# Kernel tuning notes

Hardware: AMD Instinct MI355X
Metric: run time of the kernel (lower is better)

The kernel has to match this reference:

```python
import jax, jax.numpy as jnp
import numpy as np

B, HN, N1, DIM = 4096, 16, 192, 256
EPS = 1e-5


def _xavier(key, fan_out, fan_in):
    limit = np.sqrt(6.0 / (fan_in + fan_out)).astype(np.float32)
    return jax.random.uniform(key, (fan_out, fan_in), jnp.float32, -limit, limit)


def setup_inputs() -> dict:
    key = jax.random.key(0)
    k_rgb, k_tir, k_idx, k_w1, k_w2 = jax.random.split(key, 5)
    attn_rgb_weight = jax.random.uniform(k_rgb, (B, HN, N1), jnp.float32)
    attn_tir_weight = jax.random.uniform(k_tir, (B, HN, N1), jnp.float32)
    # unique, sorted indices per batch into [0, DIM) (scatter with duplicate
    # indices is nondeterministic in torch, so we keep them unique)
    idx = jax.vmap(lambda k: jax.random.permutation(k, DIM)[:N1])(
        jax.random.split(k_idx, B))
    global_index_s = jnp.sort(idx, axis=-1).astype(jnp.int32)
    return {
        "attn_rgb_weight": attn_rgb_weight,
        "attn_tir_weight": attn_tir_weight,
        "global_index_s": global_index_s,
        "ln_g": jnp.ones((2 * DIM,), jnp.float32),
        "ln_b": jnp.zeros((2 * DIM,), jnp.float32),
        "W1": _xavier(k_w1, DIM, 2 * DIM),   # Linear(512 -> 256), torch (out,in)
        "b1": jnp.zeros((DIM,), jnp.float32),
        "W2": _xavier(k_w2, 2 * DIM, DIM),   # Linear(256 -> 512)
        "b2": jnp.zeros((2 * DIM,), jnp.float32),
    }


def reference(attn_rgb_weight, attn_tir_weight, global_index_s,
              ln_g, ln_b, W1, b1, W2, b2):
    b, hn, n1 = attn_rgb_weight.shape
    idx = global_index_s[:, None, :]                     # [B, 1, N1]
    bi = jnp.arange(b)[:, None, None]                    # [B, 1, 1]
    hi = jnp.arange(hn)[None, :, None]                   # [1, hn, 1]
    # scatter sparse attention weights into dense [B, hn, DIM] buffers
    vex_rgb = jnp.zeros((b, hn, DIM), attn_rgb_weight.dtype)
    vex_rgb = vex_rgb.at[bi, hi, idx].set(attn_rgb_weight)
    vex_tir = jnp.zeros((b, hn, DIM), attn_tir_weight.dtype)
    vex_tir = vex_tir.at[bi, hi, idx].set(attn_tir_weight)
    vex = jnp.concatenate([vex_rgb, vex_tir], axis=-1)   # [B, hn, 2*DIM]
    # LayerNorm(2*DIM) -> Linear -> ReLU -> Linear -> Sigmoid
    mu = jnp.mean(vex, axis=-1, keepdims=True)
    var = jnp.mean(jnp.square(vex - mu), axis=-1, keepdims=True)
    x = (vex - mu) * jax.lax.rsqrt(var + EPS) * ln_g + ln_b
    h = jax.nn.relu(jnp.einsum('bhe,de->bhd', x, W1) + b1)
    o = jax.nn.sigmoid(jnp.einsum('bhd,ed->bhe', h, W2) + b2)  # [B, hn, 2*DIM]
    # gather back via index
    idx_full = jnp.broadcast_to(idx, (b, hn, n1))
    out_rgb = jnp.take_along_axis(o[:, :, :DIM], idx_full, axis=-1)
    out_tir = jnp.take_along_axis(o[:, :, DIM:], idx_full, axis=-1)
    return (out_rgb, out_tir)
```

## Files before the change

kernel.cpp:

```cpp
#include <hip/hip_runtime.h>
#include <stdint.h>

#define NJ 192
#define OUT_HALF 12582912

#define XS 520
#define HS 264
#define OS 516

#define W1_OFF 33280
#define H_OFF  49664
#define ARENA  66560

typedef __attribute__((ext_vector_type(4))) float    f32x4;
typedef __attribute__((ext_vector_type(4))) int      i32x4;
typedef __attribute__((ext_vector_type(4))) uint32_t u32x4;
typedef __attribute__((ext_vector_type(8))) short    bf16x8;

__device__ __forceinline__ float bf2f(short u) {
    union { float f; uint32_t i; } c;
    c.i = ((uint32_t)(uint16_t)u) << 16;
    return c.f;
}
__device__ __forceinline__ uint32_t cvt_pk_bf16(float lo, float hi) {
    uint32_t r;
    asm("v_cvt_pk_bf16_f32 %0, %1, %2" : "=v"(r) : "v"(lo), "v"(hi));
    return r;
}
__device__ __forceinline__ void gload16(const void* g, void* l) {
    __builtin_amdgcn_global_load_lds(
        (const __attribute__((address_space(1))) uint32_t*)g,
        (__attribute__((address_space(3))) uint32_t*)l, 16, 0, 0);
}

__global__ __launch_bounds__(256)
void pack_weights(const float* __restrict__ W1, const float* __restrict__ W2,
                  short* __restrict__ ws) {
    int id = blockIdx.x * 256 + threadIdx.x;
    const float* src;
    short* dst;
    if (id < 16384) {
        int c = id >> 10, u = id & 1023;
        int nt = u >> 6, lane = u & 63;
        src = W1 + (nt * 16 + (lane & 15)) * 512 + c * 32 + (lane >> 4) * 8;
        dst = ws + id * 8;
    } else {
        int id2 = id - 16384;
        int c = id2 >> 11, u = id2 & 2047;
        int nt = u >> 6, lane = u & 63;
        src = W2 + (nt * 16 + (lane & 15)) * 256 + c * 32 + (lane >> 4) * 8;
        dst = ws + 131072 + id2 * 8;
    }
    f32x4 a = *(const f32x4*)src;
    f32x4 b = *(const f32x4*)(src + 4);
    u32x4 o;
    o[0] = cvt_pk_bf16(a[0], a[1]);
    o[1] = cvt_pk_bf16(a[2], a[3]);
    o[2] = cvt_pk_bf16(b[0], b[1]);
    o[3] = cvt_pk_bf16(b[2], b[3]);
    *(u32x4*)dst = o;
}

__global__ __launch_bounds__(512, 4)
void fused_mlp(const float* __restrict__ rgb,
               const float* __restrict__ tir,
               const int*  __restrict__ gidx,
               const float* __restrict__ ln_g,
               const float* __restrict__ ln_b,
               const short* __restrict__ P1,
               const float* __restrict__ b1,
               const short* __restrict__ P2,
               const float* __restrict__ b2,
               float* __restrict__ out)
{
    __shared__ __attribute__((aligned(16))) char arena[ARENA];
    short* sX  = (short*)arena;
    short* sW1 = (short*)(arena + W1_OFF);
    short* sH  = (short*)(arena + H_OFF);
    short* sW2 = (short*)arena;
    float* sO  = (float*)arena;

    const int tid  = threadIdx.x;
    const int blk  = blockIdx.x;
    const int row0 = blk * 32;
    const int b0   = blk * 2;
    const int wave = tid >> 6;
    const int lane = tid & 63;
    const int lr   = lane & 15;
    const int quad = lane >> 4;
    const int mw   = wave & 1;
    const int nw   = wave >> 1;

    const char* P1b = (const char*)P1;
    const char* P2b = (const char*)P2;
    char* w1dst = arena + W1_OFF + wave * 1024;
    char* w2dst = arena + wave * 1024;

    #pragma unroll
    for (int k = 0; k < 2; ++k)
        gload16(P1b + (k * 512 + tid) * 16, w1dst + k * 8192);

    {
        u32x4* xz = (u32x4*)sX;
        for (int u = tid; u < 2080; u += 512) xz[u] = (u32x4){0u, 0u, 0u, 0u};
    }
    __syncthreads();

    i32x4 ivs[3];
    #pragma unroll
    for (int it = 0; it < 3; ++it) {
        int p = (it * 512 + tid) * 4;
        int r = p / NJ;
        int j = p - r * NJ;
        ivs[it] = *(const i32x4*)&gidx[(b0 + (r >> 4)) * NJ + j];
        f32x4 vr = *(const f32x4*)&rgb[(row0 + r) * NJ + j];
        f32x4 vt = *(const f32x4*)&tir[(row0 + r) * NJ + j];
        short* xr = sX + r * XS;
        #pragma unroll
        for (int e = 0; e < 4; ++e) {
            uint32_t pk = cvt_pk_bf16(vr[e], vt[e]);
            xr[ivs[it][e]]       = (short)pk;
            xr[256 + ivs[it][e]] = (short)(pk >> 16);
        }
    }
    __syncthreads();

    {
        int r = tid >> 4, sub = tid & 15;
        short* xr = sX + r * XS + sub * 32;
        float s = 0.f, ss = 0.f;
        #pragma unroll
        for (int t = 0; t < 4; ++t) {
            bf16x8 v8 = *(bf16x8*)(xr + t * 8);
            #pragma unroll
            for (int e = 0; e < 8; ++e) { float v = bf2f(v8[e]); s += v; ss += v * v; }
        }
        s += __shfl_xor(s, 1, 16);  ss += __shfl_xor(ss, 1, 16);
        s += __shfl_xor(s, 2, 16);  ss += __shfl_xor(ss, 2, 16);
        s += __shfl_xor(s, 4, 16);  ss += __shfl_xor(ss, 4, 16);
        s += __shfl_xor(s, 8, 16);  ss += __shfl_xor(ss, 8, 16);
        float mu  = s * (1.f / 512.f);
        float var = ss * (1.f / 512.f) - mu * mu;
        float rs  = rsqrtf(var + 1e-5f);
        const float* gp = ln_g + sub * 32;
        const float* bp = ln_b + sub * 32;
        #pragma unroll
        for (int t = 0; t < 4; ++t) {
            bf16x8 v8 = *(bf16x8*)(xr + t * 8);
            f32x4 g0 = *(const f32x4*)(gp + t * 8);
            f32x4 g1 = *(const f32x4*)(gp + t * 8 + 4);
            f32x4 c0 = *(const f32x4*)(bp + t * 8);
            f32x4 c1 = *(const f32x4*)(bp + t * 8 + 4);
            float y0 = (bf2f(v8[0]) - mu) * rs * g0[0] + c0[0];
            float y1 = (bf2f(v8[1]) - mu) * rs * g0[1] + c0[1];
            float y2 = (bf2f(v8[2]) - mu) * rs * g0[2] + c0[2];
            float y3 = (bf2f(v8[3]) - mu) * rs * g0[3] + c0[3];
            float y4 = (bf2f(v8[4]) - mu) * rs * g1[0] + c1[0];
            float y5 = (bf2f(v8[5]) - mu) * rs * g1[1] + c1[1];
            float y6 = (bf2f(v8[6]) - mu) * rs * g1[2] + c1[2];
            float y7 = (bf2f(v8[7]) - mu) * rs * g1[3] + c1[3];
            u32x4 w;
            w[0] = cvt_pk_bf16(y0, y1);
            w[1] = cvt_pk_bf16(y2, y3);
            w[2] = cvt_pk_bf16(y4, y5);
            w[3] = cvt_pk_bf16(y6, y7);
            *(u32x4*)(xr + t * 8) = w;
        }
    }

    f32x4 acc1[4];
    #pragma unroll
    for (int i = 0; i < 4; ++i) acc1[i] = (f32x4){0.f, 0.f, 0.f, 0.f};

    const short* xrow   = sX + (mw * 16 + lr) * XS + quad * 8;
    const short* wfrag1 = sW1 + (nw * 4 * 64 + lane) * 8;

    for (int c = 0; c < 16; ++c) {
        __syncthreads();
        bf16x8 a = *(const bf16x8*)(xrow + c * 32);
        #pragma unroll
        for (int i = 0; i < 4; ++i) {
            bf16x8 b = *(const bf16x8*)(wfrag1 + i * 512);
            acc1[i] = __builtin_amdgcn_mfma_f32_16x16x32_bf16(a, b, acc1[i], 0, 0, 0);
        }
        __syncthreads();
        if (c < 15) {
            #pragma unroll
            for (int k = 0; k < 2; ++k)
                gload16(P1b + (c + 1) * 16384 + (k * 512 + tid) * 16, w1dst + k * 8192);
        }
    }

    #pragma unroll
    for (int k = 0; k < 4; ++k)
        gload16(P2b + (k * 512 + tid) * 16, w2dst + k * 8192);

    #pragma unroll
    for (int i = 0; i < 4; ++i) {
        int col = (nw * 4 + i) * 16 + lr;
        float bias = b1[col];
        #pragma unroll
        for (int rr = 0; rr < 4; ++rr) {
            int row = mw * 16 + quad * 4 + rr;
            float h = fmaxf(acc1[i][rr] + bias, 0.f);
            sH[row * HS + col] = (short)cvt_pk_bf16(h, h);
        }
    }

    f32x4 acc2[8];
    #pragma unroll
    for (int i = 0; i < 8; ++i) acc2[i] = (f32x4){0.f, 0.f, 0.f, 0.f};

    const short* hrow   = sH + (mw * 16 + lr) * HS + quad * 8;
    const short* wfrag2 = sW2 + (nw * 8 * 64 + lane) * 8;

    for (int c = 0; c < 8; ++c) {
        __syncthreads();
        bf16x8 a = *(const bf16x8*)(hrow + c * 32);
        #pragma unroll
        for (int i = 0; i < 8; ++i) {
            bf16x8 b = *(const bf16x8*)(wfrag2 + i * 512);
            acc2[i] = __builtin_amdgcn_mfma_f32_16x16x32_bf16(a, b, acc2[i], 0, 0, 0);
        }
        __syncthreads();
        if (c < 7) {
            #pragma unroll
            for (int k = 0; k < 4; ++k)
                gload16(P2b + (c + 1) * 32768 + (k * 512 + tid) * 16, w2dst + k * 8192);
        }
    }

    #pragma unroll
    for (int i = 0; i < 8; ++i) {
        int col = (nw * 8 + i) * 16 + lr;
        float bias = b2[col];
        #pragma unroll
        for (int rr = 0; rr < 4; ++rr) {
            int row = mw * 16 + quad * 4 + rr;
            float x = acc2[i][rr] + bias;
            sO[row * OS + col] = 1.f / (1.f + __expf(-x));
        }
    }
    __syncthreads();

    #pragma unroll
    for (int it = 0; it < 3; ++it) {
        int p = (it * 512 + tid) * 4;
        int r = p / NJ;
        int j = p - r * NJ;
        const float* orow = sO + r * OS;
        f32x4 vr, vt;
        #pragma unroll
        for (int e = 0; e < 4; ++e) {
            vr[e] = orow[ivs[it][e]];
            vt[e] = orow[256 + ivs[it][e]];
        }
        *(f32x4*)&out[(row0 + r) * NJ + j]            = vr;
        *(f32x4*)&out[OUT_HALF + (row0 + r) * NJ + j] = vt;
    }
}

extern "C" void kernel_launch(void* const* d_in, const int* in_sizes, int n_in,
                              void* d_out, int out_size, void* d_ws, size_t ws_size,
                              hipStream_t stream) {
    const float* rgb  = (const float*)d_in[0];
    const float* tir  = (const float*)d_in[1];
    const int*   gidx = (const int*)d_in[2];
    const float* ln_g = (const float*)d_in[3];
    const float* ln_b = (const float*)d_in[4];
    const float* W1   = (const float*)d_in[5];
    const float* b1   = (const float*)d_in[6];
    const float* W2   = (const float*)d_in[7];
    const float* b2   = (const float*)d_in[8];
    float* out = (float*)d_out;
    short* wsp = (short*)d_ws;

    pack_weights<<<128, 256, 0, stream>>>(W1, W2, wsp);
    fused_mlp<<<2048, 512, 0, stream>>>(rgb, tir, gidx, ln_g, ln_b,
                                        wsp, b1, wsp + 131072, b2, out);
}
```

Measured before the change: 277.4 us.

## Fold LayerNorm into W1, double rows per block, register-cache X fragments

The LayerNorm affine (gamma, beta) and bias b1 are folded into the packed W1 and precomputed per-column vectors, so the kernel only computes per-row mean/rstd, applies them after the first GEMM, and skips the normalize-and-rewrite pass over X. Each block now handles 64 rows instead of 32, halving how often each block streams the weights, and holds the A fragments for GEMM1 in registers. Weight tiles are double-buffered in 8KB/16KB slots, and the W2 prefetch overlaps the tail of GEMM1. Output columns are interleaved rgb/tir so the gather reads float2 pairs. This raises register pressure (16 A fragments plus 16 accumulators) and computes the LN statistics from fp32 inputs before the bf16 rounding.

```diff
diff --git a/kernel.cpp b/kernel.cpp
--- a/kernel.cpp
+++ b/kernel.cpp
@@ -6,22 +6,22 @@
 
 #define XS 520
 #define HS 264
-#define OS 516
-
-#define W1_OFF 33280
-#define H_OFF  49664
-#define ARENA  66560
+#define OSD 516
+
+#define SLOTB  16384
+#define H_OFF  33280
+#define STAT_OFF 67072
+#define ARENA  67584
 
 typedef __attribute__((ext_vector_type(4))) float    f32x4;
+typedef __attribute__((ext_vector_type(2))) float    f32x2;
 typedef __attribute__((ext_vector_type(4))) int      i32x4;
 typedef __attribute__((ext_vector_type(4))) uint32_t u32x4;
 typedef __attribute__((ext_vector_type(8))) short    bf16x8;
 
-__device__ __forceinline__ float bf2f(short u) {
-    union { float f; uint32_t i; } c;
-    c.i = ((uint32_t)(uint16_t)u) << 16;
-    return c.f;
-}
+__device__ float g_u1[256];
+__device__ float g_v1[256];
+
 __device__ __forceinline__ uint32_t cvt_pk_bf16(float lo, float hi) {
     uint32_t r;
     asm("v_cvt_pk_bf16_f32 %0, %1, %2" : "=v"(r) : "v"(lo), "v"(hi));
@@ -35,228 +35,263 @@
 
 __global__ __launch_bounds__(256)
 void pack_weights(const float* __restrict__ W1, const float* __restrict__ W2,
-                  short* __restrict__ ws) {
+                  const float* __restrict__ ln_g, const float* __restrict__ ln_b,
+                  const float* __restrict__ b1, short* __restrict__ ws) {
+    if (blockIdx.x == 128) {
+        int d = threadIdx.x;
+        float u = b1[d], v = 0.f;
+        const float* wr = W1 + d * 512;
+        for (int e = 0; e < 512; e += 4) {
+            f32x4 w4 = *(const f32x4*)(wr + e);
+            f32x4 g4 = *(const f32x4*)(ln_g + e);
+            f32x4 l4 = *(const f32x4*)(ln_b + e);
+            #pragma unroll
+            for (int t = 0; t < 4; ++t) { v += w4[t] * g4[t]; u += w4[t] * l4[t]; }
+        }
+        g_u1[d] = u; g_v1[d] = v;
+        return;
+    }
     int id = blockIdx.x * 256 + threadIdx.x;
-    const float* src;
-    short* dst;
     if (id < 16384) {
-        int c = id >> 10, u = id & 1023;
-        int nt = u >> 6, lane = u & 63;
-        src = W1 + (nt * 16 + (lane & 15)) * 512 + c * 32 + (lane >> 4) * 8;
-        dst = ws + id * 8;
+        int u8 = id >> 9, w = id & 511;
+        int c = u8 >> 1, h = u8 & 1;
+        int t2 = w >> 6, lane = w & 63;
+        int nt = 2 * t2 + h;
+        int row = nt * 16 + (lane & 15);
+        int k0 = c * 16 + ((lane >> 4) << 2);
+        f32x4 a  = *(const f32x4*)(W1 + row * 512 + k0);
+        f32x4 b  = *(const f32x4*)(W1 + row * 512 + 256 + k0);
+        f32x4 ga = *(const f32x4*)(ln_g + k0);
+        f32x4 gb = *(const f32x4*)(ln_g + 256 + k0);
+        u32x4 o;
+        #pragma unroll
+        for (int t = 0; t < 4; ++t) o[t] = cvt_pk_bf16(a[t] * ga[t], b[t] * gb[t]);
+        *(u32x4*)(ws + id * 8) = o;
     } else {
         int id2 = id - 16384;
-        int c = id2 >> 11, u = id2 & 2047;
-        int nt = u >> 6, lane = u & 63;
-        src = W2 + (nt * 16 + (lane & 15)) * 256 + c * 32 + (lane >> 4) * 8;
-        dst = ws + 131072 + id2 * 8;
-    }
-    f32x4 a = *(const f32x4*)src;
-    f32x4 b = *(const f32x4*)(src + 4);
-    u32x4 o;
-    o[0] = cvt_pk_bf16(a[0], a[1]);
-    o[1] = cvt_pk_bf16(a[2], a[3]);
-    o[2] = cvt_pk_bf16(b[0], b[1]);
-    o[3] = cvt_pk_bf16(b[2], b[3]);
-    *(u32x4*)dst = o;
+        int u16 = id2 >> 10, w = id2 & 1023;
+        int c = u16 >> 1, h = u16 & 1;
+        int t2 = w >> 6, lane = w & 63;
+        int nt = 2 * t2 + h;
+        int rp = nt * 16 + (lane & 15);
+        int orow = (rp >> 1) + (rp & 1) * 256;
+        int k0 = c * 32 + ((lane >> 4) << 3);
+        f32x4 a = *(const f32x4*)(W2 + orow * 256 + k0);
+        f32x4 b = *(const f32x4*)(W2 + orow * 256 + k0 + 4);
+        u32x4 o;
+        o[0] = cvt_pk_bf16(a[0], a[1]);
+        o[1] = cvt_pk_bf16(a[2], a[3]);
+        o[2] = cvt_pk_bf16(b[0], b[1]);
+        o[3] = cvt_pk_bf16(b[2], b[3]);
+        *(u32x4*)(ws + 131072 + id2 * 8) = o;
+    }
 }
 
 __global__ __launch_bounds__(512, 4)
 void fused_mlp(const float* __restrict__ rgb,
                const float* __restrict__ tir,
                const int*  __restrict__ gidx,
-               const float* __restrict__ ln_g,
-               const float* __restrict__ ln_b,
                const short* __restrict__ P1,
-               const float* __restrict__ b1,
                const short* __restrict__ P2,
                const float* __restrict__ b2,
                float* __restrict__ out)
 {
     __shared__ __attribute__((aligned(16))) char arena[ARENA];
-    short* sX  = (short*)arena;
-    short* sW1 = (short*)(arena + W1_OFF);
-    short* sH  = (short*)(arena + H_OFF);
-    short* sW2 = (short*)arena;
-    float* sO  = (float*)arena;
+    short* sX    = (short*)arena;
+    short* sH    = (short*)(arena + H_OFF);
+    float* sStat = (float*)(arena + STAT_OFF);
+    float* sO    = (float*)arena;
 
     const int tid  = threadIdx.x;
     const int blk  = blockIdx.x;
-    const int row0 = blk * 32;
-    const int b0   = blk * 2;
+    const int row0 = blk * 64;
+    const int b0   = blk * 4;
     const int wave = tid >> 6;
     const int lane = tid & 63;
     const int lr   = lane & 15;
     const int quad = lane >> 4;
-    const int mw   = wave & 1;
-    const int nw   = wave >> 1;
+    const int mw   = wave & 3;
+    const int nw   = wave >> 2;
 
     const char* P1b = (const char*)P1;
     const char* P2b = (const char*)P2;
-    char* w1dst = arena + W1_OFF + wave * 1024;
-    char* w2dst = arena + wave * 1024;
-
-    #pragma unroll
-    for (int k = 0; k < 2; ++k)
-        gload16(P1b + (k * 512 + tid) * 16, w1dst + k * 8192);
 
     {
-        u32x4* xz = (u32x4*)sX;
-        for (int u = tid; u < 2080; u += 512) xz[u] = (u32x4){0u, 0u, 0u, 0u};
-    }
-    __syncthreads();
-
-    i32x4 ivs[3];
-    #pragma unroll
-    for (int it = 0; it < 3; ++it) {
-        int p = (it * 512 + tid) * 4;
-        int r = p / NJ;
-        int j = p - r * NJ;
-        ivs[it] = *(const i32x4*)&gidx[(b0 + (r >> 4)) * NJ + j];
-        f32x4 vr = *(const f32x4*)&rgb[(row0 + r) * NJ + j];
-        f32x4 vt = *(const f32x4*)&tir[(row0 + r) * NJ + j];
-        short* xr = sX + r * XS;
-        #pragma unroll
-        for (int e = 0; e < 4; ++e) {
-            uint32_t pk = cvt_pk_bf16(vr[e], vt[e]);
-            xr[ivs[it][e]]       = (short)pk;
-            xr[256 + ivs[it][e]] = (short)(pk >> 16);
+        uint32_t* xd = (uint32_t*)sX;
+        #pragma unroll
+        for (int i = 0; i < 8; ++i) {
+            int u = i * 512 + tid;
+            int r = u >> 6, g = u & 63;
+            *(u32x4*)(xd + r * 260 + g * 4) = (u32x4){0u, 0u, 0u, 0u};
         }
     }
     __syncthreads();
 
     {
-        int r = tid >> 4, sub = tid & 15;
-        short* xr = sX + r * XS + sub * 32;
+        int r = tid >> 3, sub = tid & 7;
+        int j0 = sub * 24;
+        uint32_t* xdw = (uint32_t*)(sX + r * XS);
+        const int*   gp = gidx + (b0 + (r >> 4)) * NJ + j0;
+        const float* rp = rgb + (row0 + r) * NJ + j0;
+        const float* tp = tir + (row0 + r) * NJ + j0;
         float s = 0.f, ss = 0.f;
         #pragma unroll
-        for (int t = 0; t < 4; ++t) {
-            bf16x8 v8 = *(bf16x8*)(xr + t * 8);
-            #pragma unroll
-            for (int e = 0; e < 8; ++e) { float v = bf2f(v8[e]); s += v; ss += v * v; }
-        }
-        s += __shfl_xor(s, 1, 16);  ss += __shfl_xor(ss, 1, 16);
-        s += __shfl_xor(s, 2, 16);  ss += __shfl_xor(ss, 2, 16);
-        s += __shfl_xor(s, 4, 16);  ss += __shfl_xor(ss, 4, 16);
-        s += __shfl_xor(s, 8, 16);  ss += __shfl_xor(ss, 8, 16);
+        for (int q = 0; q < 6; ++q) {
+            i32x4 iv = *(const i32x4*)(gp + q * 4);
+            f32x4 vr = *(const f32x4*)(rp + q * 4);
+            f32x4 vt = *(const f32x4*)(tp + q * 4);
+            #pragma unroll
+            for (int e = 0; e < 4; ++e) {
+                s  += vr[e] + vt[e];
+                ss += vr[e] * vr[e] + vt[e] * vt[e];
+                xdw[iv[e]] = cvt_pk_bf16(vr[e], vt[e]);
+            }
+        }
+        s  += __shfl_xor(s, 1, 8);  ss += __shfl_xor(ss, 1, 8);
+        s  += __shfl_xor(s, 2, 8);  ss += __shfl_xor(ss, 2, 8);
+        s  += __shfl_xor(s, 4, 8);  ss += __shfl_xor(ss, 4, 8);
         float mu  = s * (1.f / 512.f);
         float var = ss * (1.f / 512.f) - mu * mu;
         float rs  = rsqrtf(var + 1e-5f);
-        const float* gp = ln_g + sub * 32;
-        const float* bp = ln_b + sub * 32;
-        #pragma unroll
-        for (int t = 0; t < 4; ++t) {
-            bf16x8 v8 = *(bf16x8*)(xr + t * 8);
-            f32x4 g0 = *(const f32x4*)(gp + t * 8);
-            f32x4 g1 = *(const f32x4*)(gp + t * 8 + 4);
-            f32x4 c0 = *(const f32x4*)(bp + t * 8);
-            f32x4 c1 = *(const f32x4*)(bp + t * 8 + 4);
-            float y0 = (bf2f(v8[0]) - mu) * rs * g0[0] + c0[0];
-            float y1 = (bf2f(v8[1]) - mu) * rs * g0[1] + c0[1];
-            float y2 = (bf2f(v8[2]) - mu) * rs * g0[2] + c0[2];
-            float y3 = (bf2f(v8[3]) - mu) * rs * g0[3] + c0[3];
-            float y4 = (bf2f(v8[4]) - mu) * rs * g1[0] + c1[0];
-            float y5 = (bf2f(v8[5]) - mu) * rs * g1[1] + c1[1];
-            float y6 = (bf2f(v8[6]) - mu) * rs * g1[2] + c1[2];
-            float y7 = (bf2f(v8[7]) - mu) * rs * g1[3] + c1[3];
-            u32x4 w;
-            w[0] = cvt_pk_bf16(y0, y1);
-            w[1] = cvt_pk_bf16(y2, y3);
-            w[2] = cvt_pk_bf16(y4, y5);
-            w[3] = cvt_pk_bf16(y6, y7);
-            *(u32x4*)(xr + t * 8) = w;
-        }
-    }
-
-    f32x4 acc1[4];
-    #pragma unroll
-    for (int i = 0; i < 4; ++i) acc1[i] = (f32x4){0.f, 0.f, 0.f, 0.f};
-
-    const short* xrow   = sX + (mw * 16 + lr) * XS + quad * 8;
-    const short* wfrag1 = sW1 + (nw * 4 * 64 + lane) * 8;
-
-    for (int c = 0; c < 16; ++c) {
+        if (sub == 0) { sStat[2 * r] = rs; sStat[2 * r + 1] = mu * rs; }
+    }
+    __syncthreads();
+
+    bf16x8 a1[16];
+    {
+        const short* xr = sX + (mw * 16 + lr) * XS + quad * 8;
+        #pragma unroll
+        for (int c = 0; c < 16; ++c) a1[c] = *(const bf16x8*)(xr + c * 32);
+    }
+    __syncthreads();
+
+    gload16(P1b + 0 * 8192 + tid * 16, arena + 0       + wave * 1024);
+    gload16(P1b + 1 * 8192 + tid * 16, arena + SLOTB   + wave * 1024);
+    __syncthreads();
+
+    f32x4 acc1[8];
+    #pragma unroll
+    for (int i = 0; i < 8; ++i) acc1[i] = (f32x4){0.f, 0.f, 0.f, 0.f};
+
+    const short* wb = (const short*)arena + lane * 8;
+
+    #pragma unroll
+    for (int j = 0; j < 32; ++j) {
+        const int c = j >> 1, h = j & 1;
+        bf16x8 w0 = *(const bf16x8*)(wb + (j & 1) * 8192 + (nw * 4 + 0) * 512);
+        bf16x8 w1 = *(const bf16x8*)(wb + (j & 1) * 8192 + (nw * 4 + 1) * 512);
+        bf16x8 w2 = *(const bf16x8*)(wb + (j & 1) * 8192 + (nw * 4 + 2) * 512);
+        bf16x8 w3 = *(const bf16x8*)(wb + (j & 1) * 8192 + (nw * 4 + 3) * 512);
         __syncthreads();
-        bf16x8 a = *(const bf16x8*)(xrow + c * 32);
-        #pragma unroll
-        for (int i = 0; i < 4; ++i) {
-            bf16x8 b = *(const bf16x8*)(wfrag1 + i * 512);
-            acc1[i] = __builtin_amdgcn_mfma_f32_16x16x32_bf16(a, b, acc1[i], 0, 0, 0);
-        }
+        if (j <= 29) {
+            gload16(P1b + (j + 2) * 8192 + tid * 16,
+                    arena + (j & 1) * SLOTB + wave * 1024);
+        } else {
+            const int u = j - 30;
+            gload16(P2b + u * 16384 + tid * 16,
+                    arena + u * SLOTB + wave * 1024);
+            gload16(P2b + u * 16384 + 8192 + tid * 16,
+                    arena + u * SLOTB + 8192 + wave * 1024);
+        }
+        acc1[0 + h] = __builtin_amdgcn_mfma_f32_16x16x32_bf16(a1[c], w0, acc1[0 + h], 0, 0, 0);
+        acc1[2 + h] = __builtin_amdgcn_mfma_f32_16x16x32_bf16(a1[c], w1, acc1[2 + h], 0, 0, 0);
+        acc1[4 + h] = __builtin_amdgcn_mfma_f32_16x16x32_bf16(a1[c], w2, acc1[4 + h], 0, 0, 0);
+        acc1[6 + h] = __builtin_amdgcn_mfma_f32_16x16x32_bf16(a1[c], w3, acc1[6 + h], 0, 0, 0);
+    }
+
+    {
+        const int baserow = mw * 16 + quad * 4;
+        float rsv[4], mrs[4];
+        #pragma unroll
+        for (int rr = 0; rr < 4; ++rr) {
+            rsv[rr] = sStat[2 * (baserow + rr)];
+            mrs[rr] = sStat[2 * (baserow + rr) + 1];
+        }
+        #pragma unroll
+        for (int i = 0; i < 8; ++i) {
+            int col = (nw * 8 + i) * 16 + lr;
+            float u1c = g_u1[col], v1c = g_v1[col];
+            #pragma unroll
+            for (int rr = 0; rr < 4; ++rr) {
+                float hh = rsv[rr] * acc1[i][rr] + (u1c - mrs[rr] * v1c);
+                hh = fmaxf(hh, 0.f);
+                sH[(baserow + rr) * HS + col] = (short)cvt_pk_bf16(hh, hh);
+            }
+        }
+    }
+    __syncthreads();
+
+    f32x4 acc2[16];
+    #pragma unroll
+    for (int i = 0; i < 16; ++i) acc2[i] = (f32x4){0.f, 0.f, 0.f, 0.f};
+
+    const short* hrow = sH + (mw * 16 + lr) * HS + quad * 8;
+
+    #pragma unroll
+    for (int j = 0; j < 16; ++j) {
+        const int c = j >> 1, h = j & 1;
+        bf16x8 a = *(const bf16x8*)(hrow + c * 32);
+        bf16x8 w0 = *(const bf16x8*)(wb + (j & 1) * 8192 + (nw * 8 + 0) * 512);
+        bf16x8 w1 = *(const bf16x8*)(wb + (j & 1) * 8192 + (nw * 8 + 1) * 512);
+        bf16x8 w2 = *(const bf16x8*)(wb + (j & 1) * 8192 + (nw * 8 + 2) * 512);
+        bf16x8 w3 = *(const bf16x8*)(wb + (j & 1) * 8192 + (nw * 8 + 3) * 512);
+        bf16x8 w4 = *(const bf16x8*)(wb + (j & 1) * 8192 + (nw * 8 + 4) * 512);
+        bf16x8 w5 = *(const bf16x8*)(wb + (j & 1) * 8192 + (nw * 8 + 5) * 512);
+        bf16x8 w6 = *(const bf16x8*)(wb + (j & 1) * 8192 + (nw * 8 + 6) * 512);
+        bf16x8 w7 = *(const bf16x8*)(wb + (j & 1) * 8192 + (nw * 8 + 7) * 512);
         __syncthreads();
-        if (c < 15) {
-            #pragma unroll
-            for (int k = 0; k < 2; ++k)
-                gload16(P1b + (c + 1) * 16384 + (k * 512 + tid) * 16, w1dst + k * 8192);
-        }
-    }
-
-    #pragma unroll
-    for (int k = 0; k < 4; ++k)
-        gload16(P2b + (k * 512 + tid) * 16, w2dst + k * 8192);
-
-    #pragma unroll
-    for (int i = 0; i < 4; ++i) {
-        int col = (nw * 4 + i) * 16 + lr;
-        float bias = b1[col];
-        #pragma unroll
-        for (int rr = 0; rr < 4; ++rr) {
-            int row = mw * 16 + quad * 4 + rr;
-            float h = fmaxf(acc1[i][rr] + bias, 0.f);
-            sH[row * HS + col] = (short)cvt_pk_bf16(h, h);
-        }
-    }
-
-    f32x4 acc2[8];
-    #pragma unroll
-    for (int i = 0; i < 8; ++i) acc2[i] = (f32x4){0.f, 0.f, 0.f, 0.f};
-
-    const short* hrow   = sH + (mw * 16 + lr) * HS + quad * 8;
-    const short* wfrag2 = sW2 + (nw * 8 * 64 + lane) * 8;
-
-    for (int c = 0; c < 8; ++c) {
+        if (j <= 13) {
+            gload16(P2b + (j + 2) * 16384 + tid * 16,
+                    arena + (j & 1) * SLOTB + wave * 1024);
+            gload16(P2b + (j + 2) * 16384 + 8192 + tid * 16,
+                    arena + (j & 1) * SLOTB + 8192 + wave * 1024);
+        }
+        acc2[0  + h] = __builtin_amdgcn_mfma_f32_16x16x32_bf16(a, w0, acc2[0  + h], 0, 0, 0);
+        acc2[2  + h] = __builtin_amdgcn_mfma_f32_16x16x32_bf16(a, w1, acc2[2  + h], 0, 0, 0);
+        acc2[4  + h] = __builtin_amdgcn_mfma_f32_16x16x32_bf16(a, w2, acc2[4  + h], 0, 0, 0);
+        acc2[6  + h] = __builtin_amdgcn_mfma_f32_16x16x32_bf16(a, w3, acc2[6  + h], 0, 0, 0);
+        acc2[8  + h] = __builtin_amdgcn_mfma_f32_16x16x32_bf16(a, w4, acc2[8  + h], 0, 0, 0);
+        acc2[10 + h] = __builtin_amdgcn_mfma_f32_16x16x32_bf16(a, w5, acc2[10 + h], 0, 0, 0);
+        acc2[12 + h] = __builtin_amdgcn_mfma_f32_16x16x32_bf16(a, w6, acc2[12 + h], 0, 0, 0);
+        acc2[14 + h] = __builtin_amdgcn_mfma_f32_16x16x32_bf16(a, w7, acc2[14 + h], 0, 0, 0);
+    }
+
+    const int prow = mw >> 1;
+    const int baserow2 = (mw & 1) * 16 + quad * 4;
+
+    #pragma unroll
+    for (int p = 0; p < 2; ++p) {
+        if (prow == p) {
+            #pragma unroll
+            for (int i = 0; i < 16; ++i) {
+                int colp = (nw * 16 + i) * 16 + lr;
+                float b2v = b2[(colp >> 1) + (colp & 1) * 256];
+                #pragma unroll
+                for (int rr = 0; rr < 4; ++rr) {
+                    float x = acc2[i][rr] + b2v;
+                    sO[(baserow2 + rr) * OSD + colp] = 1.f / (1.f + __expf(-x));
+                }
+            }
+        }
         __syncthreads();
-        bf16x8 a = *(const bf16x8*)(hrow + c * 32);
-        #pragma unroll
-        for (int i = 0; i < 8; ++i) {
-            bf16x8 b = *(const bf16x8*)(wfrag2 + i * 512);
-            acc2[i] = __builtin_amdgcn_mfma_f32_16x16x32_bf16(a, b, acc2[i], 0, 0, 0);
-        }
-        __syncthreads();
-        if (c < 7) {
-            #pragma unroll
-            for (int k = 0; k < 4; ++k)
-                gload16(P2b + (c + 1) * 32768 + (k * 512 + tid) * 16, w2dst + k * 8192);
-        }
-    }
-
-    #pragma unroll
-    for (int i = 0; i < 8; ++i) {
-        int col = (nw * 8 + i) * 16 + lr;
-        float bias = b2[col];
-        #pragma unroll
-        for (int rr = 0; rr < 4; ++rr) {
-            int row = mw * 16 + quad * 4 + rr;
-            float x = acc2[i][rr] + bias;
-            sO[row * OS + col] = 1.f / (1.f + __expf(-x));
-        }
-    }
-    __syncthreads();
-
-    #pragma unroll
-    for (int it = 0; it < 3; ++it) {
-        int p = (it * 512 + tid) * 4;
-        int r = p / NJ;
-        int j = p - r * NJ;
-        const float* orow = sO + r * OS;
-        f32x4 vr, vt;
-        #pragma unroll
-        for (int e = 0; e < 4; ++e) {
-            vr[e] = orow[ivs[it][e]];
-            vt[e] = orow[256 + ivs[it][e]];
-        }
-        *(f32x4*)&out[(row0 + r) * NJ + j]            = vr;
-        *(f32x4*)&out[OUT_HALF + (row0 + r) * NJ + j] = vt;
+        #pragma unroll
+        for (int it = 0; it < 3; ++it) {
+            int q4 = (it * 512 + tid) * 4;
+            int rl = q4 / NJ;
+            int jj = q4 - rl * NJ;
+            int r  = p * 32 + rl;
+            i32x4 iv = *(const i32x4*)(gidx + (b0 + (r >> 4)) * NJ + jj);
+            const float* orow = sO + rl * OSD;
+            f32x4 vr, vt;
+            #pragma unroll
+            for (int e = 0; e < 4; ++e) {
+                f32x2 pr = *(const f32x2*)(orow + 2 * iv[e]);
+                vr[e] = pr[0]; vt[e] = pr[1];
+            }
+            *(f32x4*)&out[(row0 + r) * NJ + jj]            = vr;
+            *(f32x4*)&out[OUT_HALF + (row0 + r) * NJ + jj] = vt;
+        }
+        if (p == 0) __syncthreads();
     }
 }
 
@@ -275,7 +310,7 @@
     float* out = (float*)d_out;
     short* wsp = (short*)d_ws;
 
-    pack_weights<<<128, 256, 0, stream>>>(W1, W2, wsp);
-    fused_mlp<<<2048, 512, 0, stream>>>(rgb, tir, gidx, ln_g, ln_b,
-                                        wsp, b1, wsp + 131072, b2, out);
-}
+    pack_weights<<<129, 256, 0, stream>>>(W1, W2, ln_g, ln_b, b1, wsp);
+    fused_mlp<<<1024, 512, 0, stream>>>(rgb, tir, gidx,
+                                        wsp, wsp + 131072, b2, out);
+}
```

New measurement: 270.0 us. 2.7% less time.
